# Kernel optimization log

Hardware: AMD Instinct MI355X
Metric: run time of the kernel (lower is better)

Reference implementation:

```python
import jax, jax.numpy as jnp
import numpy as np

EMBED_DIM = 1024
NUM_HEADS = 16
HEAD_DIM = EMBED_DIM // NUM_HEADS
B, S = 4, 2048


def setup_inputs() -> dict:
    key = jax.random.key(0)
    ks = jax.random.split(key, 12)
    s = 1.0 / np.sqrt(EMBED_DIM)
    inp = {
        'q': jax.random.normal(ks[0], (B, S, EMBED_DIM), jnp.float32),
        'k': jax.random.normal(ks[1], (B, S, EMBED_DIM), jnp.float32),
        'v': jax.random.normal(ks[2], (B, S, EMBED_DIM), jnp.float32),
        'mask': jnp.tril(jnp.ones((S, S), jnp.int32))[None, None],  # [1,1,S,S] causal
        'Wq': jax.random.normal(ks[3], (EMBED_DIM, EMBED_DIM), jnp.float32) * s,
        'bq': jax.random.normal(ks[4], (EMBED_DIM,), jnp.float32) * s,
        'Wk': jax.random.normal(ks[5], (EMBED_DIM, EMBED_DIM), jnp.float32) * s,
        'bk': jax.random.normal(ks[6], (EMBED_DIM,), jnp.float32) * s,
        'Wv': jax.random.normal(ks[7], (EMBED_DIM, EMBED_DIM), jnp.float32) * s,
        'bv': jax.random.normal(ks[8], (EMBED_DIM,), jnp.float32) * s,
        'Wo': jax.random.normal(ks[9], (EMBED_DIM, EMBED_DIM), jnp.float32) * s,
        'bo': jax.random.normal(ks[10], (EMBED_DIM,), jnp.float32) * s,
    }
    return inp


def _split(x):
    b, s, _ = x.shape
    return x.reshape(b, s, NUM_HEADS, HEAD_DIM).transpose(0, 2, 1, 3)  # [b,h,s,d]


def reference(q, k, v, mask, Wq, bq, Wk, bk, Wv, bv, Wo, bo):
    # torch Linear: x @ W.T + b
    Q = _split(q @ Wq.T + bq)
    K = _split(k @ Wk.T + bk)
    V = _split(v @ Wv.T + bv)
    scores = jnp.einsum('bhqd,bhkd->bhqk', Q, K) / np.sqrt(HEAD_DIM).astype(np.float32)
    scores = jnp.where(mask == 0, jnp.float32(-1e9), scores)
    attn = jax.nn.softmax(scores, axis=-1)  # dropout p=0.0 -> identity
    out = jnp.einsum('bhqk,bhkd->bhqd', attn, V)
    out = out.transpose(0, 2, 1, 3).reshape(q.shape[0], q.shape[1], EMBED_DIM)
    return out @ Wo.T + bo
```

## Files before the change

### kernel.cpp

```cpp
#include <hip/hip_runtime.h>

#define SEQ   2048
#define EMB   1024
#define NH    16
#define HD    64
#define BATCH 4

typedef __attribute__((ext_vector_type(8))) short short8;
typedef __attribute__((ext_vector_type(4))) float floatx4;
typedef __attribute__((ext_vector_type(4))) uint uintx4;

static __device__ __forceinline__ ushort f2bf_rne(float x) {
  unsigned u = __float_as_uint(x);
  unsigned r = u + 0x7FFFu + ((u >> 16) & 1u);
  return (ushort)(r >> 16);
}
static __device__ __forceinline__ float bf2f(ushort h) {
  return __uint_as_float(((unsigned)h) << 16);
}

static __device__ __forceinline__ uint pk_bf16(float a, float b) {
  uint r;
  asm("v_cvt_pk_bf16_f32 %0, %1, %2" : "=v"(r) : "v"(a), "v"(b));
  return r;
}
static __device__ __forceinline__ void split_pair(float a, float b, uint& h,
                                                  uint& l) {
  h = pk_bf16(a, b);
  const float ha = __uint_as_float(h << 16);
  const float hb = __uint_as_float(h & 0xFFFF0000u);
  l = pk_bf16(a - ha, b - hb);
}

static __device__ __forceinline__ void load16(const void* g, void* l) {
  __builtin_amdgcn_global_load_lds(
      (const __attribute__((address_space(1))) unsigned int*)g,
      (__attribute__((address_space(3))) unsigned int*)l, 16, 0, 0);
}

static __device__ __forceinline__ int swz_off(int row, int kg) {
  return (row >> 1) * 128 + (((row & 1) << 2) + (kg ^ ((row >> 1) & 3))) * 16;
}

static __device__ __forceinline__ void stage_tile(const ushort* __restrict__ g,
                                                  int row0, int k0,
                                                  ushort* lds, int t) {
#pragma unroll
  for (int i = 0; i < 2; ++i) {
    const int slot = t + i * 256;
    const int line = slot >> 3, s = slot & 7;
    const int row = line * 2 + (s >> 2);
    const int c = (s & 3) ^ (line & 3);
    load16(g + (size_t)(row0 + row) * EMB + k0 + c * 8, lds + slot * 8);
  }
}

__global__ __launch_bounds__(256) void wconv_kernel(const float* __restrict__ W,
                                                    ushort* __restrict__ Yh,
                                                    ushort* __restrict__ Yl) {
  const int i = (blockIdx.x * 256 + threadIdx.x) * 8;
  const float4 a = *(const float4*)(W + i);
  const float4 b = *(const float4*)(W + i + 4);
  const float xv[8] = {a.x, a.y, a.z, a.w, b.x, b.y, b.z, b.w};
  uintx4 H, L;
#pragma unroll
  for (int j = 0; j < 4; ++j) {
    uint h, l;
    split_pair(xv[2 * j], xv[2 * j + 1], h, l);
    H[j] = h;
    L[j] = l;
  }
  *(uintx4*)&Yh[i] = H;
  *(uintx4*)&Yl[i] = L;
}

template <int MODE, bool PREA, bool PREB>
__global__ __launch_bounds__(256) void proj_mfma_kernel(
    const float* __restrict__ X, const ushort* __restrict__ Xh,
    const ushort* __restrict__ Xl, const float* __restrict__ W,
    const ushort* __restrict__ Wh, const ushort* __restrict__ Wl,
    const float* __restrict__ bias, float* __restrict__ Yf,
    ushort* __restrict__ Yh, ushort* __restrict__ Yl) {
  __shared__ ushort Ahi[PREA ? 128 * 32 : 128 * 40];
  __shared__ ushort Alo[PREA ? 128 * 32 : 128 * 40];
  __shared__ ushort Bhi[PREB ? 128 * 32 : 128 * 40];
  __shared__ ushort Blo[PREB ? 128 * 32 : 128 * 40];

  const int t = threadIdx.x;
  const int lane = t & 63, wave = t >> 6;
  const int m0 = blockIdx.y * 128, n0 = blockIdx.x * 128;
  const int wm = (wave >> 1) * 64, wn = (wave & 1) * 64;
  const int fr = lane & 15, kg = lane >> 4;

  floatx4 acc[4][4];
#pragma unroll
  for (int i = 0; i < 4; ++i)
#pragma unroll
    for (int j = 0; j < 4; ++j)
#pragma unroll
      for (int r = 0; r < 4; ++r) acc[i][j][r] = 0.f;

#pragma unroll 1
  for (int k0 = 0; k0 < EMB; k0 += 32) {
    __syncthreads();
    if constexpr (PREA) {
      stage_tile(Xh, m0, k0, Ahi, t);
      stage_tile(Xl, m0, k0, Alo, t);
    } else {
#pragma unroll
      for (int i = 0; i < 4; ++i) {
        const int f = t + 256 * i;
        const int row = f >> 3, kq = f & 7;
        const float4 a =
            *(const float4*)(X + (size_t)(m0 + row) * EMB + k0 + kq * 4);
        uint h0, l0, h1, l1;
        split_pair(a.x, a.y, h0, l0);
        split_pair(a.z, a.w, h1, l1);
        uint2 hp, lp;
        hp.x = h0; hp.y = h1;
        lp.x = l0; lp.y = l1;
        *(uint2*)&Ahi[row * 40 + kq * 4] = hp;
        *(uint2*)&Alo[row * 40 + kq * 4] = lp;
      }
    }
    if constexpr (PREB) {
      stage_tile(Wh, n0, k0, Bhi, t);
      stage_tile(Wl, n0, k0, Blo, t);
    } else {
#pragma unroll
      for (int i = 0; i < 4; ++i) {
        const int f = t + 256 * i;
        const int row = f >> 3, kq = f & 7;
        const float4 b =
            *(const float4*)(W + (size_t)(n0 + row) * EMB + k0 + kq * 4);
        uint h0, l0, h1, l1;
        split_pair(b.x, b.y, h0, l0);
        split_pair(b.z, b.w, h1, l1);
        uint2 hp, lp;
        hp.x = h0; hp.y = h1;
        lp.x = l0; lp.y = l1;
        *(uint2*)&Bhi[row * 40 + kq * 4] = hp;
        *(uint2*)&Blo[row * 40 + kq * 4] = lp;
      }
    }
    if constexpr (PREA || PREB) asm volatile("s_waitcnt vmcnt(0)");
    __syncthreads();

    short8 bhv[4], blv[4];
#pragma unroll
    for (int nf = 0; nf < 4; ++nf) {
      const int row = wn + nf * 16 + fr;
      if constexpr (PREB) {
        const int off = swz_off(row, kg);
        bhv[nf] = *(const short8*)((const char*)Bhi + off);
        blv[nf] = *(const short8*)((const char*)Blo + off);
      } else {
        bhv[nf] = *(const short8*)&Bhi[row * 40 + kg * 8];
        blv[nf] = *(const short8*)&Blo[row * 40 + kg * 8];
      }
    }
#pragma unroll
    for (int mf = 0; mf < 4; ++mf) {
      const int arow = wm + mf * 16 + fr;
      short8 ah, al;
      if constexpr (PREA) {
        const int off = swz_off(arow, kg);
        ah = *(const short8*)((const char*)Ahi + off);
        al = *(const short8*)((const char*)Alo + off);
      } else {
        ah = *(const short8*)&Ahi[arow * 40 + kg * 8];
        al = *(const short8*)&Alo[arow * 40 + kg * 8];
      }
#pragma unroll
      for (int nf = 0; nf < 4; ++nf) {
        acc[mf][nf] = __builtin_amdgcn_mfma_f32_16x16x32_bf16(ah, bhv[nf],
                                                              acc[mf][nf], 0, 0, 0);
        acc[mf][nf] = __builtin_amdgcn_mfma_f32_16x16x32_bf16(ah, blv[nf],
                                                              acc[mf][nf], 0, 0, 0);
        acc[mf][nf] = __builtin_amdgcn_mfma_f32_16x16x32_bf16(al, bhv[nf],
                                                              acc[mf][nf], 0, 0, 0);
      }
    }
  }

  const int rg = lane >> 4;
#pragma unroll
  for (int nf = 0; nf < 4; ++nf) {
    const int n = n0 + wn + nf * 16 + fr;
    const float bb = bias[n];
    if (MODE == 2) {
      const int hh = n >> 6, d = n & 63;
#pragma unroll
      for (int mf = 0; mf < 4; ++mf) {
        const int mb = m0 + wm + mf * 16 + rg * 4;
        const int b = mb >> 11, s = mb & (SEQ - 1);
        uint h0, l0, h1, l1;
        split_pair(acc[mf][nf][0] + bb, acc[mf][nf][1] + bb, h0, l0);
        split_pair(acc[mf][nf][2] + bb, acc[mf][nf][3] + bb, h1, l1);
        uint2 hp, lp;
        hp.x = h0; hp.y = h1;
        lp.x = l0; lp.y = l1;
        const int idx = (b * NH + hh) * (HD * SEQ) + d * SEQ + s;
        *(uint2*)&Yh[idx] = hp;
        *(uint2*)&Yl[idx] = lp;
      }
    } else {
#pragma unroll
      for (int mf = 0; mf < 4; ++mf) {
#pragma unroll
        for (int r = 0; r < 4; ++r) {
          const int m = m0 + wm + mf * 16 + rg * 4 + r;
          float val = acc[mf][nf][r] + bb;
          if (MODE == 3) {
            Yf[(size_t)m * EMB + n] = val;
          } else {
            if (MODE == 0) val *= 0.125f;
            const int hh = n >> 6, d = n & 63;
            const int b = m >> 11, s = m & (SEQ - 1);
            const int idx = ((b * NH + hh) * SEQ + s) * HD + d;
            const ushort h = f2bf_rne(val);
            Yh[idx] = h;
            Yl[idx] = f2bf_rne(val - bf2f(h));
          }
        }
      }
    }
  }
}

template <bool SPLITOUT>
__global__ __launch_bounds__(256, 2) void attn_mfma_kernel(
    const ushort* __restrict__ Qh, const ushort* __restrict__ Ql,
    const ushort* __restrict__ Kh, const ushort* __restrict__ Kl,
    const ushort* __restrict__ Vth, const ushort* __restrict__ Vtl,
    float* __restrict__ O, ushort* __restrict__ Oh, ushort* __restrict__ Ol) {
  __shared__ __align__(16) ushort KHs[2][64 * 64], KLs[2][64 * 64];
  __shared__ __align__(16) ushort VHs[2][64 * 64], VLs[2][64 * 64];

  const int bh = blockIdx.x;
  const int qtA = blockIdx.y;
  const int qtB = 15 - qtA;
  const int t = threadIdx.x;
  const int lane = t & 63, wave = t >> 6;
  const int fr = lane & 15, kg = lane >> 4;
  const int base = bh * (SEQ * HD);
  const int r8 = lane >> 3, c8 = lane & 7;

  const int q00[2] = {qtA * 128 + wave * 32, qtB * 128 + wave * 32};
  const int ext[2] = {(q00[0] + 95) >> 6, (q00[1] + 95) >> 6};
  const int nkt = 2 * qtB + 2;

  short8 qfh[2][2][2], qfl[2][2][2];
#pragma unroll
  for (int g = 0; g < 2; ++g)
#pragma unroll
    for (int mf = 0; mf < 2; ++mf)
#pragma unroll
      for (int ks = 0; ks < 2; ++ks) {
        const int idx = base + (q00[g] + mf * 16 + fr) * HD + ks * 32 + kg * 8;
        qfh[g][mf][ks] = *(const short8*)&Qh[idx];
        qfl[g][mf][ks] = *(const short8*)&Ql[idx];
      }

  floatx4 oacc[2][2][4];
  float m_run[2][2], l_run[2][2];
#pragma unroll
  for (int g = 0; g < 2; ++g)
#pragma unroll
    for (int mf = 0; mf < 2; ++mf) {
#pragma unroll
      for (int nf = 0; nf < 4; ++nf)
#pragma unroll
        for (int r = 0; r < 4; ++r) oacc[g][mf][nf][r] = 0.f;
      m_run[g][mf] = -INFINITY;
      l_run[g][mf] = 0.f;
    }

  auto stage = [&](int kt, int b) {
#pragma unroll
    for (int i = 0; i < 2; ++i) {
      const int lrow = wave * 16 + i * 8;
      const int row = lrow + r8;
      const int sw = (c8 ^ (row & 7)) << 3;
      const int gk = base + (kt * 64 + row) * HD + sw;
      const int gv = base + row * SEQ + kt * 64 + sw;
      load16(Kh + gk, (char*)KHs + b * 8192 + lrow * 128);
      load16(Kl + gk, (char*)KLs + b * 8192 + lrow * 128);
      load16(Vth + gv, (char*)VHs + b * 8192 + lrow * 128);
      load16(Vtl + gv, (char*)VLs + b * 8192 + lrow * 128);
    }
  };

  stage(0, 0);
  asm volatile("s_waitcnt vmcnt(0)");
  __syncthreads();

#pragma unroll 1
  for (int kt = 0; kt < nkt; ++kt) {
    const int cur = kt & 1;
    if (kt + 1 < nkt) stage(kt + 1, cur ^ 1);
    const int c0 = kt * 64;
    const int kb = cur * 8192;

#pragma unroll
    for (int g = 0; g < 2; ++g) {
      if (kt < ext[g]) {
        const int q0 = q00[g];

        floatx4 s2[2][4];
#pragma unroll
        for (int mf = 0; mf < 2; ++mf)
#pragma unroll
          for (int nf = 0; nf < 4; ++nf)
#pragma unroll
            for (int r = 0; r < 4; ++r) s2[mf][nf][r] = 0.f;

#pragma unroll
        for (int ksd = 0; ksd < 2; ++ksd)
#pragma unroll
          for (int nf = 0; nf < 4; ++nf) {
            const int kr =
                32 * (nf >> 1) + 8 * (fr >> 2) + 4 * (nf & 1) + (fr & 3);
            const int byo = kb + kr * 128 + (((ksd * 4 + kg) ^ (kr & 7)) << 4);
            const short8 kh = *(const short8*)((const char*)KHs + byo);
            const short8 kl = *(const short8*)((const char*)KLs + byo);
#pragma unroll
            for (int mf = 0; mf < 2; ++mf) {
              s2[mf][nf] = __builtin_amdgcn_mfma_f32_16x16x32_bf16(
                  kh, qfh[g][mf][ksd], s2[mf][nf], 0, 0, 0);
              s2[mf][nf] = __builtin_amdgcn_mfma_f32_16x16x32_bf16(
                  kh, qfl[g][mf][ksd], s2[mf][nf], 0, 0, 0);
              s2[mf][nf] = __builtin_amdgcn_mfma_f32_16x16x32_bf16(
                  kl, qfh[g][mf][ksd], s2[mf][nf], 0, 0, 0);
            }
          }

        if (c0 + 63 > q0) {
#pragma unroll
          for (int mf = 0; mf < 2; ++mf)
#pragma unroll
            for (int nf = 0; nf < 4; ++nf)
#pragma unroll
              for (int r = 0; r < 4; ++r) {
                const int col =
                    c0 + 32 * (nf >> 1) + 8 * kg + 4 * (nf & 1) + r;
                const int row = q0 + mf * 16 + fr;
                if (col > row) s2[mf][nf][r] = -1e9f;
              }
        }

        float pmv[2];
#pragma unroll
        for (int mf = 0; mf < 2; ++mf) {
          float pm = s2[mf][0][0];
#pragma unroll
          for (int nf = 0; nf < 4; ++nf)
#pragma unroll
            for (int r = 0; r < 4; ++r) pm = fmaxf(pm, s2[mf][nf][r]);
          pm = fmaxf(pm, __shfl_xor(pm, 16));
          pm = fmaxf(pm, __shfl_xor(pm, 32));
          pmv[mf] = pm;
        }
        float alpha2[2] = {1.f, 1.f};
        const bool grow = !__all((pmv[0] <= m_run[g][0] + 8.f) &&
                                 (pmv[1] <= m_run[g][1] + 8.f));
        if (grow) {
#pragma unroll
          for (int mf = 0; mf < 2; ++mf) {
            const float mnew = fmaxf(m_run[g][mf], pmv[mf]);
            alpha2[mf] = __expf(m_run[g][mf] - mnew);
            m_run[g][mf] = mnew;
          }
#pragma unroll
          for (int mf = 0; mf < 2; ++mf)
#pragma unroll
            for (int r = 0; r < 4; ++r) {
              const float a = __shfl(alpha2[mf], (kg * 4 + r) | (lane & 48));
#pragma unroll
              for (int nf = 0; nf < 4; ++nf) oacc[g][mf][nf][r] *= a;
            }
        }
#pragma unroll
        for (int mf = 0; mf < 2; ++mf) {
          const float mm = m_run[g][mf];
          float sum = 0.f;
#pragma unroll
          for (int nf = 0; nf < 4; ++nf)
#pragma unroll
            for (int r = 0; r < 4; ++r) {
              const float p = __expf(s2[mf][nf][r] - mm);
              s2[mf][nf][r] = p;
              sum += p;
            }
          sum += __shfl_xor(sum, 16);
          sum += __shfl_xor(sum, 32);
          l_run[g][mf] = l_run[g][mf] * alpha2[mf] + sum;
        }

        short8 pah[2][2], pal[2][2];
#pragma unroll
        for (int mf = 0; mf < 2; ++mf)
#pragma unroll
          for (int ks = 0; ks < 2; ++ks) {
            uintx4 H, L;
#pragma unroll
            for (int jj = 0; jj < 4; ++jj) {
              const int nfi = 2 * ks + (jj >> 1);
              uint h, l;
              split_pair(s2[mf][nfi][(2 * jj) & 3], s2[mf][nfi][(2 * jj + 1) & 3],
                         h, l);
              H[jj] = h;
              L[jj] = l;
            }
            pah[mf][ks] = *(short8*)&H;
            pal[mf][ks] = *(short8*)&L;
          }

#pragma unroll
        for (int ks = 0; ks < 2; ++ks)
#pragma unroll
          for (int nf = 0; nf < 4; ++nf) {
            const int d = nf * 16 + fr;
            const int byo = kb + d * 128 + (((ks * 4 + kg) ^ (d & 7)) << 4);
            const short8 vh = *(const short8*)((const char*)VHs + byo);
            const short8 vl = *(const short8*)((const char*)VLs + byo);
#pragma unroll
            for (int mf = 0; mf < 2; ++mf) {
              oacc[g][mf][nf] = __builtin_amdgcn_mfma_f32_16x16x32_bf16(
                  pah[mf][ks], vh, oacc[g][mf][nf], 0, 0, 0);
              oacc[g][mf][nf] = __builtin_amdgcn_mfma_f32_16x16x32_bf16(
                  pah[mf][ks], vl, oacc[g][mf][nf], 0, 0, 0);
              oacc[g][mf][nf] = __builtin_amdgcn_mfma_f32_16x16x32_bf16(
                  pal[mf][ks], vh, oacc[g][mf][nf], 0, 0, 0);
            }
          }
      }
    }

    asm volatile("s_waitcnt vmcnt(0)");
    __syncthreads();
  }

  const int b = bh >> 4, hsel = bh & 15;
#pragma unroll
  for (int g = 0; g < 2; ++g)
#pragma unroll
    for (int mf = 0; mf < 2; ++mf)
#pragma unroll
      for (int r = 0; r < 4; ++r) {
        const float lv = __shfl(l_run[g][mf], (kg * 4 + r) | (lane & 48));
        const float inv = 1.f / lv;
        const int grow2 = q00[g] + mf * 16 + kg * 4 + r;
        const int rowbase = (b * SEQ + grow2) * EMB + hsel * HD;
#pragma unroll
        for (int nf = 0; nf < 4; ++nf) {
          const float val = oacc[g][mf][nf][r] * inv;
          const int idx = rowbase + nf * 16 + fr;
          if constexpr (SPLITOUT) {
            const ushort hh = f2bf_rne(val);
            Oh[idx] = hh;
            Ol[idx] = f2bf_rne(val - bf2f(hh));
          } else {
            O[idx] = val;
          }
        }
      }
}

extern "C" void kernel_launch(void* const* d_in, const int* in_sizes, int n_in,
                              void* d_out, int out_size, void* d_ws,
                              size_t ws_size, hipStream_t stream) {
  const float* q = (const float*)d_in[0];
  const float* k = (const float*)d_in[1];
  const float* v = (const float*)d_in[2];
  const float* Wq = (const float*)d_in[4];
  const float* bq = (const float*)d_in[5];
  const float* Wk = (const float*)d_in[6];
  const float* bk = (const float*)d_in[7];
  const float* Wv = (const float*)d_in[8];
  const float* bv = (const float*)d_in[9];
  const float* Wo = (const float*)d_in[10];
  const float* bo = (const float*)d_in[11];
  float* out = (float*)d_out;

  const size_t E = (size_t)BATCH * SEQ * EMB;
  const size_t WE = (size_t)EMB * EMB;
  ushort* us = (ushort*)d_ws;
  ushort* Qh = us;
  ushort* Ql = us + E;
  ushort* Kh = us + 2 * E;
  ushort* Kl = us + 3 * E;
  ushort* Vth = us + 4 * E;
  ushort* Vtl = us + 5 * E;

  const dim3 pgrid(EMB / 128, (BATCH * SEQ) / 128);
  const dim3 agrid(BATCH * NH, 8);
  const dim3 blk(256);
  const int wgrid = (int)(WE / 8 / 256);

  if (ws_size >= 8 * E * sizeof(ushort)) {
    ushort* W3 = us + 6 * E;
    ushort* Wqh = W3, *Wql = W3 + WE;
    ushort* Wkh = W3 + 2 * WE, *Wkl = W3 + 3 * WE;
    ushort* Wvh = W3 + 4 * WE, *Wvl = W3 + 5 * WE;
    ushort* AOh = us + 6 * E, *AOl = us + 7 * E;
    ushort* Woh = us, *Wol = us + WE;

    wconv_kernel<<<wgrid, blk, 0, stream>>>(Wq, Wqh, Wql);
    wconv_kernel<<<wgrid, blk, 0, stream>>>(Wk, Wkh, Wkl);
    wconv_kernel<<<wgrid, blk, 0, stream>>>(Wv, Wvh, Wvl);
    proj_mfma_kernel<0, false, true><<<pgrid, blk, 0, stream>>>(
        q, nullptr, nullptr, nullptr, Wqh, Wql, bq, nullptr, Qh, Ql);
    proj_mfma_kernel<1, false, true><<<pgrid, blk, 0, stream>>>(
        k, nullptr, nullptr, nullptr, Wkh, Wkl, bk, nullptr, Kh, Kl);
    proj_mfma_kernel<2, false, true><<<pgrid, blk, 0, stream>>>(
        v, nullptr, nullptr, nullptr, Wvh, Wvl, bv, nullptr, Vth, Vtl);
    attn_mfma_kernel<true><<<agrid, blk, 0, stream>>>(Qh, Ql, Kh, Kl, Vth, Vtl,
                                                      nullptr, AOh, AOl);
    wconv_kernel<<<wgrid, blk, 0, stream>>>(Wo, Woh, Wol);
    proj_mfma_kernel<3, true, true><<<pgrid, blk, 0, stream>>>(
        nullptr, AOh, AOl, nullptr, Woh, Wol, bo, out, nullptr, nullptr);
  } else if (ws_size >= (6 * E + 6 * WE) * sizeof(ushort)) {
    ushort* W3 = us + 6 * E;
    ushort* Wqh = W3, *Wql = W3 + WE;
    ushort* Wkh = W3 + 2 * WE, *Wkl = W3 + 3 * WE;
    ushort* Wvh = W3 + 4 * WE, *Wvl = W3 + 5 * WE;
    ushort* AOh = (ushort*)d_out, *AOl = AOh + E;
    ushort* Woh = us, *Wol = us + WE;
    float* PO = (float*)(us + 2 * E);

    wconv_kernel<<<wgrid, blk, 0, stream>>>(Wq, Wqh, Wql);
    wconv_kernel<<<wgrid, blk, 0, stream>>>(Wk, Wkh, Wkl);
    wconv_kernel<<<wgrid, blk, 0, stream>>>(Wv, Wvh, Wvl);
    proj_mfma_kernel<0, false, true><<<pgrid, blk, 0, stream>>>(
        q, nullptr, nullptr, nullptr, Wqh, Wql, bq, nullptr, Qh, Ql);
    proj_mfma_kernel<1, false, true><<<pgrid, blk, 0, stream>>>(
        k, nullptr, nullptr, nullptr, Wkh, Wkl, bk, nullptr, Kh, Kl);
    proj_mfma_kernel<2, false, true><<<pgrid, blk, 0, stream>>>(
        v, nullptr, nullptr, nullptr, Wvh, Wvl, bv, nullptr, Vth, Vtl);
    attn_mfma_kernel<true><<<agrid, blk, 0, stream>>>(Qh, Ql, Kh, Kl, Vth, Vtl,
                                                      nullptr, AOh, AOl);
    wconv_kernel<<<wgrid, blk, 0, stream>>>(Wo, Woh, Wol);
    proj_mfma_kernel<3, true, true><<<pgrid, blk, 0, stream>>>(
        nullptr, AOh, AOl, nullptr, Woh, Wol, bo, PO, nullptr, nullptr);
    hipError_t e1 = hipMemcpyAsync(out, PO, E * sizeof(float),
                                   hipMemcpyDeviceToDevice, stream);
    (void)e1;
  } else {
    float* AO = out;
    float* PO = (float*)d_ws;
    proj_mfma_kernel<0, false, false><<<pgrid, blk, 0, stream>>>(
        q, nullptr, nullptr, Wq, nullptr, nullptr, bq, nullptr, Qh, Ql);
    proj_mfma_kernel<1, false, false><<<pgrid, blk, 0, stream>>>(
        k, nullptr, nullptr, Wk, nullptr, nullptr, bk, nullptr, Kh, Kl);
    proj_mfma_kernel<2, false, false><<<pgrid, blk, 0, stream>>>(
        v, nullptr, nullptr, Wv, nullptr, nullptr, bv, nullptr, Vth, Vtl);
    attn_mfma_kernel<false><<<agrid, blk, 0, stream>>>(
        Qh, Ql, Kh, Kl, Vth, Vtl, AO, nullptr, nullptr);
    proj_mfma_kernel<3, false, false><<<pgrid, blk, 0, stream>>>(
        AO, nullptr, nullptr, Wo, nullptr, nullptr, bo, PO, nullptr, nullptr);
    hipError_t e2 = hipMemcpyAsync(out, PO, E * sizeof(float),
                                   hipMemcpyDeviceToDevice, stream);
    (void)e2;
  }
}
```

Before: 378.6 us.

## Double-buffer projection GEMM shared tiles and raise wave priority around attention MFMAs

In the projection GEMM, whenever either operand is pre-split into bf16 hi/lo, shared-memory tiles are now double-buffered. The global loads for the next k-step are issued before computing on the current buffer, which removes one barrier per iteration and overlaps loads with MFMA work. Shared memory per block doubles in that case, which may lower occupancy. Separately, the attention kernel wraps its QK and PV MFMA blocks in s_setprio(1)/s_setprio(0) so that waves issuing matrix ops are scheduled ahead of the others.

```diff
diff --git a/kernel.cpp b/kernel.cpp
--- a/kernel.cpp
+++ b/kernel.cpp
@@ -81,10 +81,12 @@
     const ushort* __restrict__ Wh, const ushort* __restrict__ Wl,
     const float* __restrict__ bias, float* __restrict__ Yf,
     ushort* __restrict__ Yh, ushort* __restrict__ Yl) {
-  __shared__ ushort Ahi[PREA ? 128 * 32 : 128 * 40];
-  __shared__ ushort Alo[PREA ? 128 * 32 : 128 * 40];
-  __shared__ ushort Bhi[PREB ? 128 * 32 : 128 * 40];
-  __shared__ ushort Blo[PREB ? 128 * 32 : 128 * 40];
+  constexpr bool DBUF = (PREA || PREB);
+  constexpr int NB = DBUF ? 2 : 1;
+  constexpr int ASZ = PREA ? 128 * 32 : 128 * 40;
+  constexpr int BSZ = PREB ? 128 * 32 : 128 * 40;
+  __shared__ ushort Ahi[NB][ASZ], Alo[NB][ASZ];
+  __shared__ ushort Bhi[NB][BSZ], Blo[NB][BSZ];
 
   const int t = threadIdx.x;
   const int lane = t & 63, wave = t >> 6;
@@ -100,63 +102,62 @@
 #pragma unroll
       for (int r = 0; r < 4; ++r) acc[i][j][r] = 0.f;
 
-#pragma unroll 1
-  for (int k0 = 0; k0 < EMB; k0 += 32) {
-    __syncthreads();
-    if constexpr (PREA) {
-      stage_tile(Xh, m0, k0, Ahi, t);
-      stage_tile(Xl, m0, k0, Alo, t);
+  auto stageB = [&](int k0, int b) {
+    if constexpr (PREB) {
+      stage_tile(Wh, n0, k0, Bhi[b], t);
+      stage_tile(Wl, n0, k0, Blo[b], t);
     } else {
 #pragma unroll
       for (int i = 0; i < 4; ++i) {
         const int f = t + 256 * i;
         const int row = f >> 3, kq = f & 7;
-        const float4 a =
-            *(const float4*)(X + (size_t)(m0 + row) * EMB + k0 + kq * 4);
+        const float4 v =
+            *(const float4*)(W + (size_t)(n0 + row) * EMB + k0 + kq * 4);
         uint h0, l0, h1, l1;
-        split_pair(a.x, a.y, h0, l0);
-        split_pair(a.z, a.w, h1, l1);
+        split_pair(v.x, v.y, h0, l0);
+        split_pair(v.z, v.w, h1, l1);
         uint2 hp, lp;
         hp.x = h0; hp.y = h1;
         lp.x = l0; lp.y = l1;
-        *(uint2*)&Ahi[row * 40 + kq * 4] = hp;
-        *(uint2*)&Alo[row * 40 + kq * 4] = lp;
-      }
-    }
-    if constexpr (PREB) {
-      stage_tile(Wh, n0, k0, Bhi, t);
-      stage_tile(Wl, n0, k0, Blo, t);
+        *(uint2*)&Bhi[b][row * 40 + kq * 4] = hp;
+        *(uint2*)&Blo[b][row * 40 + kq * 4] = lp;
+      }
+    }
+  };
+  auto stageA = [&](int k0, int b) {
+    if constexpr (PREA) {
+      stage_tile(Xh, m0, k0, Ahi[b], t);
+      stage_tile(Xl, m0, k0, Alo[b], t);
     } else {
 #pragma unroll
       for (int i = 0; i < 4; ++i) {
         const int f = t + 256 * i;
         const int row = f >> 3, kq = f & 7;
-        const float4 b =
-            *(const float4*)(W + (size_t)(n0 + row) * EMB + k0 + kq * 4);
+        const float4 v =
+            *(const float4*)(X + (size_t)(m0 + row) * EMB + k0 + kq * 4);
         uint h0, l0, h1, l1;
-        split_pair(b.x, b.y, h0, l0);
-        split_pair(b.z, b.w, h1, l1);
+        split_pair(v.x, v.y, h0, l0);
+        split_pair(v.z, v.w, h1, l1);
         uint2 hp, lp;
         hp.x = h0; hp.y = h1;
         lp.x = l0; lp.y = l1;
-        *(uint2*)&Bhi[row * 40 + kq * 4] = hp;
-        *(uint2*)&Blo[row * 40 + kq * 4] = lp;
-      }
-    }
-    if constexpr (PREA || PREB) asm volatile("s_waitcnt vmcnt(0)");
-    __syncthreads();
-
+        *(uint2*)&Ahi[b][row * 40 + kq * 4] = hp;
+        *(uint2*)&Alo[b][row * 40 + kq * 4] = lp;
+      }
+    }
+  };
+  auto computeStep = [&](int cur) {
     short8 bhv[4], blv[4];
 #pragma unroll
     for (int nf = 0; nf < 4; ++nf) {
       const int row = wn + nf * 16 + fr;
       if constexpr (PREB) {
         const int off = swz_off(row, kg);
-        bhv[nf] = *(const short8*)((const char*)Bhi + off);
-        blv[nf] = *(const short8*)((const char*)Blo + off);
+        bhv[nf] = *(const short8*)((const char*)Bhi[cur] + off);
+        blv[nf] = *(const short8*)((const char*)Blo[cur] + off);
       } else {
-        bhv[nf] = *(const short8*)&Bhi[row * 40 + kg * 8];
-        blv[nf] = *(const short8*)&Blo[row * 40 + kg * 8];
+        bhv[nf] = *(const short8*)&Bhi[cur][row * 40 + kg * 8];
+        blv[nf] = *(const short8*)&Blo[cur][row * 40 + kg * 8];
       }
     }
 #pragma unroll
@@ -165,11 +166,11 @@
       short8 ah, al;
       if constexpr (PREA) {
         const int off = swz_off(arow, kg);
-        ah = *(const short8*)((const char*)Ahi + off);
-        al = *(const short8*)((const char*)Alo + off);
+        ah = *(const short8*)((const char*)Ahi[cur] + off);
+        al = *(const short8*)((const char*)Alo[cur] + off);
       } else {
-        ah = *(const short8*)&Ahi[arow * 40 + kg * 8];
-        al = *(const short8*)&Alo[arow * 40 + kg * 8];
+        ah = *(const short8*)&Ahi[cur][arow * 40 + kg * 8];
+        al = *(const short8*)&Alo[cur][arow * 40 + kg * 8];
       }
 #pragma unroll
       for (int nf = 0; nf < 4; ++nf) {
@@ -180,6 +181,33 @@
         acc[mf][nf] = __builtin_amdgcn_mfma_f32_16x16x32_bf16(al, bhv[nf],
                                                               acc[mf][nf], 0, 0, 0);
       }
+    }
+  };
+
+  if constexpr (DBUF) {
+    stageB(0, 0);
+    stageA(0, 0);
+    asm volatile("s_waitcnt vmcnt(0)");
+    __syncthreads();
+#pragma unroll 1
+    for (int k0 = 0; k0 < EMB; k0 += 32) {
+      const int cur = (k0 >> 5) & 1;
+      if (k0 + 32 < EMB) {
+        stageB(k0 + 32, cur ^ 1);
+        stageA(k0 + 32, cur ^ 1);
+      }
+      computeStep(cur);
+      asm volatile("s_waitcnt vmcnt(0)");
+      __syncthreads();
+    }
+  } else {
+#pragma unroll 1
+    for (int k0 = 0; k0 < EMB; k0 += 32) {
+      __syncthreads();
+      stageB(k0, 0);
+      stageA(k0, 0);
+      __syncthreads();
+      computeStep(0);
     }
   }
 
@@ -315,6 +343,7 @@
 #pragma unroll
             for (int r = 0; r < 4; ++r) s2[mf][nf][r] = 0.f;
 
+        __builtin_amdgcn_s_setprio(1);
 #pragma unroll
         for (int ksd = 0; ksd < 2; ++ksd)
 #pragma unroll
@@ -334,6 +363,7 @@
                   kl, qfh[g][mf][ksd], s2[mf][nf], 0, 0, 0);
             }
           }
+        __builtin_amdgcn_s_setprio(0);
 
         if (c0 + 63 > q0) {
 #pragma unroll
@@ -416,6 +446,7 @@
             pal[mf][ks] = *(short8*)&L;
           }
 
+        __builtin_amdgcn_s_setprio(1);
 #pragma unroll
         for (int ks = 0; ks < 2; ++ks)
 #pragma unroll
@@ -434,6 +465,7 @@
                   pal[mf][ks], vh, oacc[g][mf][nf], 0, 0, 0);
             }
           }
+        __builtin_amdgcn_s_setprio(0);
       }
     }
 
```

After: 369.9 us. 2.3% less time.
